# Kernel tuning notes

Hardware: AMD Instinct MI355X
Metric: run time of the kernel (lower is better)

Reference implementation:

```python
import jax, jax.numpy as jnp
import numpy as np


def setup_inputs() -> dict:
    key = jax.random.key(0)
    ks = jax.random.split(key, 12)
    B, N, Dv, E, H, V, T = 128, 196, 512, 512, 1024, 10000, 20
    s = 0.02  # small init scale for numerical stability
    f = lambda k, shp: (jax.random.normal(k, shp, jnp.float32) * s)
    return {
        "features": jax.random.normal(ks[0], (B, N, Dv), jnp.float32),
        "captions": jax.random.randint(ks[1], (B, T), 0, V),
        "W_init_h": f(ks[2], (H, Dv)),
        "W_init_c": f(ks[3], (H, Dv)),
        "W_attn_v": f(ks[4], (1, Dv)),
        "b_attn_v": jnp.zeros((1,), jnp.float32),
        "W_attn_h": f(ks[5], (1, H)),
        "b_attn_h": jnp.zeros((1,), jnp.float32),
        "embed_table": f(ks[6], (V, E)),
        "W_ih": f(ks[7], (4 * H, Dv + E)),
        "W_hh": f(ks[8], (4 * H, H)),
        "b_ih": jnp.zeros((4 * H,), jnp.float32),
        "b_hh": jnp.zeros((4 * H,), jnp.float32),
        "W_out": f(ks[9], (V, H)),
        "b_out": jnp.zeros((V,), jnp.float32),
    }


def reference(features, captions, W_init_h, W_init_c, W_attn_v, b_attn_v,
              W_attn_h, b_attn_h, embed_table, W_ih, W_hh, b_ih, b_hh,
              W_out, b_out):
    B, N, Dv = features.shape
    # _init_hidden: mean over vis_num of linear projections (division by vis_num)
    h0 = jnp.sum(jnp.einsum('bnd,hd->bnh', features, W_init_h), axis=1) / N
    c0 = jnp.sum(jnp.einsum('bnd,hd->bnh', features, W_init_c), axis=1) / N

    emb = embed_table[captions]                      # B,T,E
    emb_t_major = jnp.swapaxes(emb, 0, 1)            # T,B,E
    # visual attention logits are time-invariant; precompute once
    att_v = jnp.einsum('bnd,od->bno', features, W_attn_v) + b_attn_v  # B,N,1

    def step(carry, emb_t):
        h, c = carry
        # soft attention over vis_num locations
        att_h = (h @ W_attn_h.T + b_attn_h)[:, None, :]   # B,1,1
        alpha = jax.nn.softmax(att_v + att_h, axis=1)     # B,N,1
        ctx = jnp.sum(features * alpha, axis=1)           # B,Dv
        # single-step LSTM (PyTorch gate order: i, f, g, o)
        x = jnp.concatenate([ctx, emb_t], axis=-1)        # B,Dv+E
        gates = x @ W_ih.T + h @ W_hh.T + b_ih + b_hh     # B,4H
        i, fg, g, o = jnp.split(gates, 4, axis=-1)
        c_new = jax.nn.sigmoid(fg) * c + jax.nn.sigmoid(i) * jnp.tanh(g)
        h_new = jax.nn.sigmoid(o) * jnp.tanh(c_new)
        words = h_new @ W_out.T + b_out                   # B,V
        return (h_new, c_new), words

    _, word_space = jax.lax.scan(step, (h0, c0), emb_t_major)  # T,B,V
    # pack_padded_sequence with all-equal lengths flattens time-major -> (T*B, V)
    packed = word_space.reshape(-1, word_space.shape[-1])
    return jax.nn.log_softmax(packed, axis=1), jax.nn.softmax(packed, axis=1)
```

## Files before the change

kernel.cpp:

```cpp
#include <hip/hip_runtime.h>
#include <math.h>

#define B    128
#define NLOC 196
#define DV   512
#define EMB  512
#define HD   1024
#define VV   10000
#define TT   20
#define G4   4096
#define VPAD 10112
#define BH   (B*HD)

typedef short bf16x8 __attribute__((ext_vector_type(8)));
typedef float f32x4  __attribute__((ext_vector_type(4)));

__device__ __forceinline__ unsigned short f2bf(float x) {
    unsigned u = __builtin_bit_cast(unsigned, x);
    unsigned r = (u + 0x7fffu + ((u >> 16) & 1u)) >> 16;
    return (unsigned short)r;
}
__device__ __forceinline__ float bf2f(short s) {
    unsigned u = ((unsigned)(unsigned short)s) << 16;
    return __builtin_bit_cast(float, u);
}

__device__ __forceinline__ void gload_lds16(const void* g, void* lds) {
    __builtin_amdgcn_global_load_lds(
        (const __attribute__((address_space(1))) void*)g,
        (__attribute__((address_space(3))) void*)lds, 16, 0, 0);
}


__global__ void attv_kernel(const float* __restrict__ feat, const float* __restrict__ wv,
                            const float* __restrict__ bv, float* __restrict__ attv) {
    int row  = blockIdx.x;
    int lane = threadIdx.x;
    const float* p = feat + (size_t)row * DV;
    float s = 0.f;
    for (int k = lane; k < DV; k += 64) s += p[k] * wv[k];
    for (int off = 32; off > 0; off >>= 1) s += __shfl_down(s, off);
    if (lane == 0) attv[row] = s + bv[0];
}

__global__ void alpha_kernel(const float* __restrict__ attv, float* __restrict__ alpha) {
    int b   = blockIdx.x;
    int tid = threadIdx.x;
    __shared__ float red[256];
    float v = (tid < NLOC) ? attv[b * NLOC + tid] : -1e30f;
    red[tid] = v; __syncthreads();
    for (int s = 128; s > 0; s >>= 1) { if (tid < s) red[tid] = fmaxf(red[tid], red[tid + s]); __syncthreads(); }
    float m = red[0]; __syncthreads();
    float e = (tid < NLOC) ? expf(v - m) : 0.f;
    red[tid] = e; __syncthreads();
    for (int s = 128; s > 0; s >>= 1) { if (tid < s) red[tid] += red[tid + s]; __syncthreads(); }
    float sum = red[0];
    if (tid < NLOC) alpha[b * NLOC + tid] = e / sum;
}

__global__ void fmeanctx_kernel(const float* __restrict__ feat, const float* __restrict__ alpha,
                                short* __restrict__ fmean_b, short* __restrict__ ctx_b) {
    int idx = blockIdx.x * blockDim.x + threadIdx.x;
    if (idx >= B * DV) return;
    int b = idx / DV, d = idx % DV;
    const float* p = feat + (size_t)b * NLOC * DV + d;
    const float* a = alpha + b * NLOC;
    float sm = 0.f, sc = 0.f;
    for (int n = 0; n < NLOC; ++n) {
        float v = p[(size_t)n * DV];
        sm += v;
        sc += a[n] * v;
    }
    fmean_b[idx] = (short)f2bf(sm * (1.0f / NLOC));
    ctx_b[idx]   = (short)f2bf(sc);
}

__global__ void emb_gather_kernel(const int* __restrict__ captions, const float* __restrict__ table,
                                  short* __restrict__ emb_b) {
    size_t idx = (size_t)blockIdx.x * blockDim.x + threadIdx.x;
    if (idx >= (size_t)TT * B * EMB) return;
    int k = (int)(idx % EMB);
    int r = (int)(idx / EMB);
    int t = r / B, b = r % B;
    int cap = captions[b * TT + t];
    emb_b[idx] = (short)f2bf(table[(size_t)cap * EMB + k]);
}

__global__ void f2bf_pad_kernel(const float* __restrict__ in, short* __restrict__ out,
                                size_t n, size_t npad) {
    size_t i = (size_t)blockIdx.x * blockDim.x + threadIdx.x;
    if (i >= npad) return;
    out[i] = (i < n) ? (short)f2bf(in[i]) : (short)0;
}

__global__ void whh_perm_kernel(const float* __restrict__ in, short* __restrict__ out) {
    size_t idx = (size_t)blockIdx.x * blockDim.x + threadIdx.x;
    if (idx >= (size_t)G4 * HD) return;
    int k = (int)(idx & (HD - 1));
    int P = (int)(idx >> 10);
    int u = P >> 2, g = P & 3;
    out[idx] = (short)f2bf(in[(size_t)(g * HD + u) * HD + k]);
}

template<int BN, int WR, int WC, bool BF16OUT>
__global__ __launch_bounds__(256)
void gemm_bf16(const short* __restrict__ A, const short* __restrict__ Bw,
               void* __restrict__ C,
               const float* __restrict__ bias0, const float* __restrict__ bias1,
               int NY, int M, int N, int K, int lda, int ldb, int ldc) {
    constexpr int BM = 128;
    constexpr int BK = 32;
    constexpr int WM = BM / WR;
    constexpr int WN = BN / WC;
    constexpr int FM = WM / 16;
    constexpr int FN = WN / 16;
    __shared__ __align__(16) short As[BM * BK];
    __shared__ __align__(16) short Bs[BN * BK];
    const int tid  = threadIdx.x;
    const int wave = tid >> 6, lane = tid & 63;
    const int wr = wave / WC, wc = wave % WC;

    const int nwg = gridDim.x;
    const int qq = nwg >> 3, rr8 = nwg & 7;
    const int p = blockIdx.x;
    const int xcd = p & 7, slot = p >> 3;
    const int lwg = (xcd < rr8) ? (xcd * (qq + 1) + slot)
                                : (rr8 * (qq + 1) + (xcd - rr8) * qq + slot);
    const int m0 = (lwg % NY) * BM;
    const int n0 = (lwg / NY) * BN;
    const int laneoff = lane * 16;

    f32x4 acc[FM][FN] = {};

    for (int k0 = 0; k0 < K; k0 += BK) {
        #pragma unroll
        for (int r = 0; r < 2; ++r) {
            int o   = r * 4096 + wave * 1024 + laneoff;
            int row = o >> 6;
            int gr  = (o >> 4) & 3;
            int col = ((gr ^ ((row >> 1) & 3)) << 3);
            gload_lds16(A + (size_t)(m0 + row) * lda + k0 + col,
                        (char*)As + r * 4096 + wave * 1024);
        }
        constexpr int BBYTES = BN * BK * 2;
        if constexpr (BBYTES >= 4096) {
            #pragma unroll
            for (int r = 0; r < BBYTES / 4096; ++r) {
                int o   = r * 4096 + wave * 1024 + laneoff;
                int row = o >> 6;
                int gr  = (o >> 4) & 3;
                int col = ((gr ^ ((row >> 1) & 3)) << 3);
                gload_lds16(Bw + (size_t)(n0 + row) * ldb + k0 + col,
                            (char*)Bs + r * 4096 + wave * 1024);
            }
        } else {
            constexpr int NW = BBYTES / 1024;
            if (wave < NW) {
                int o   = wave * 1024 + laneoff;
                int row = o >> 6;
                int gr  = (o >> 4) & 3;
                int col = ((gr ^ ((row >> 1) & 3)) << 3);
                gload_lds16(Bw + (size_t)(n0 + row) * ldb + k0 + col,
                            (char*)Bs + wave * 1024);
            }
        }
        __syncthreads();

        bf16x8 a[FM], b[FN];
        const int kfrg = lane >> 4;
        #pragma unroll
        for (int i = 0; i < FM; ++i) {
            int row = wr * WM + i * 16 + (lane & 15);
            a[i] = *(const bf16x8*)&As[row * BK + ((kfrg ^ ((row >> 1) & 3)) << 3)];
        }
        #pragma unroll
        for (int j = 0; j < FN; ++j) {
            int row = wc * WN + j * 16 + (lane & 15);
            b[j] = *(const bf16x8*)&Bs[row * BK + ((kfrg ^ ((row >> 1) & 3)) << 3)];
        }
        #pragma unroll
        for (int i = 0; i < FM; ++i)
            #pragma unroll
            for (int j = 0; j < FN; ++j)
                acc[i][j] = __builtin_amdgcn_mfma_f32_16x16x32_bf16(a[i], b[j], acc[i][j], 0, 0, 0);
        __syncthreads();
    }

    #pragma unroll
    for (int i = 0; i < FM; ++i) {
        #pragma unroll
        for (int j = 0; j < FN; ++j) {
            int col = n0 + wc * WN + j * 16 + (lane & 15);
            if (col >= N) continue;
            float bv = (bias0 ? bias0[col] : 0.f) + (bias1 ? bias1[col] : 0.f);
            #pragma unroll
            for (int q = 0; q < 4; ++q) {
                int row = m0 + wr * WM + i * 16 + (lane >> 4) * 4 + q;
                if (row < M) {
                    float v = acc[i][j][q] + bv;
                    if constexpr (BF16OUT)
                        ((short*)C)[(size_t)row * ldc + col] = (short)f2bf(v);
                    else
                        ((float*)C)[(size_t)row * ldc + col] = v;
                }
            }
        }
    }
}

__global__ __launch_bounds__(256)
void gemm_k64(const short* __restrict__ A, const short* __restrict__ Bw,
              short* __restrict__ C,
              const float* __restrict__ bias0,
              int NY, int M, int N, int K, int lda, int ldb, int ldc) {
    __shared__ __align__(16) short As[128 * 64];
    __shared__ __align__(16) short Bs[128 * 64];
    const int tid  = threadIdx.x;
    const int wave = tid >> 6, lane = tid & 63;
    const int wr = wave >> 1, wc = wave & 1;

    const int nwg = gridDim.x;
    const int qq = nwg >> 3, rr8 = nwg & 7;
    const int p = blockIdx.x;
    const int xcd = p & 7, slot = p >> 3;
    const int lwg = (xcd < rr8) ? (xcd * (qq + 1) + slot)
                                : (rr8 * (qq + 1) + (xcd - rr8) * qq + slot);
    const int m0 = (lwg % NY) * 128;
    const int n0 = (lwg / NY) * 128;
    const int laneoff = lane * 16;
    const int kfrg = lane >> 4;

    f32x4 acc[4][4] = {};

    for (int k0 = 0; k0 < K; k0 += 64) {
        #pragma unroll
        for (int r = 0; r < 4; ++r) {
            int o   = r * 4096 + wave * 1024 + laneoff;
            int row = o >> 7;
            int gr  = (o >> 4) & 7;
            int col = ((gr ^ (row & 7)) << 3);
            gload_lds16(A + (size_t)(m0 + row) * lda + k0 + col,
                        (char*)As + r * 4096 + wave * 1024);
            gload_lds16(Bw + (size_t)(n0 + row) * ldb + k0 + col,
                        (char*)Bs + r * 4096 + wave * 1024);
        }
        __syncthreads();

        #pragma unroll
        for (int kh = 0; kh < 2; ++kh) {
            bf16x8 a[4], b[4];
            #pragma unroll
            for (int i = 0; i < 4; ++i) {
                int row = wr * 64 + i * 16 + (lane & 15);
                a[i] = *(const bf16x8*)&As[row * 64 + (((kh * 4 + kfrg) ^ (row & 7)) << 3)];
            }
            #pragma unroll
            for (int j = 0; j < 4; ++j) {
                int row = wc * 64 + j * 16 + (lane & 15);
                b[j] = *(const bf16x8*)&Bs[row * 64 + (((kh * 4 + kfrg) ^ (row & 7)) << 3)];
            }
            #pragma unroll
            for (int i = 0; i < 4; ++i)
                #pragma unroll
                for (int j = 0; j < 4; ++j)
                    acc[i][j] = __builtin_amdgcn_mfma_f32_16x16x32_bf16(a[i], b[j], acc[i][j], 0, 0, 0);
        }
        __syncthreads();
    }

    #pragma unroll
    for (int i = 0; i < 4; ++i) {
        #pragma unroll
        for (int j = 0; j < 4; ++j) {
            int col = n0 + wc * 64 + j * 16 + (lane & 15);
            if (col >= N) continue;
            float bv = bias0 ? bias0[col] : 0.f;
            #pragma unroll
            for (int q = 0; q < 4; ++q) {
                int row = m0 + wr * 64 + i * 16 + (lane >> 4) * 4 + q;
                if (row < M) C[(size_t)row * ldc + col] = (short)f2bf(acc[i][j][q] + bv);
            }
        }
    }
}

__global__ __launch_bounds__(256)
void lstm_step6(const short* __restrict__ Hprev, const short* __restrict__ Whh_p,
                const short* __restrict__ pre_t, const short* __restrict__ gctx_b,
                float* __restrict__ cbuf, short* __restrict__ Hnext,
                short* __restrict__ Hall_t) {
    __shared__ __align__(16) short As[64 * 512];
    __shared__ __align__(16) short Ws[32 * 512];
    __shared__ float gsm[4][64][8];
    const int tid  = threadIdx.x;
    const int lane = tid & 63, wave = tid >> 6;
    const int n0 = blockIdx.x * 32;
    const int m0 = blockIdx.y * 64;

    const int arowL = wave * 16 + (lane & 15);
    const int brow0 = lane & 15;
    const int brow1 = 16 + (lane & 15);
    const int kg    = lane >> 4;

    f32x4 acc0 = {}, acc1 = {};

    for (int h2 = 0; h2 < 2; ++h2) {
        const int k0 = h2 * 512;
        #pragma unroll
        for (int it = 0; it < 16; ++it) {
            int fg  = it * 256 + tid;
            int row = fg >> 6;
            int g   = fg & 63;
            int col = (g ^ (row & 7)) * 8;
            gload_lds16(Hprev + (size_t)(m0 + row) * HD + k0 + col,
                        (char*)As + it * 4096 + wave * 1024);
        }
        #pragma unroll
        for (int it = 0; it < 8; ++it) {
            int fg  = it * 256 + tid;
            int row = fg >> 6;
            int g   = fg & 63;
            int col = (g ^ (row & 7)) * 8;
            gload_lds16(Whh_p + (size_t)(n0 + row) * HD + k0 + col,
                        (char*)Ws + it * 4096 + wave * 1024);
        }
        __syncthreads();
        #pragma unroll
        for (int ks = 0; ks < 16; ++ks) {
            int lg = ks * 4 + kg;
            bf16x8 a  = *(const bf16x8*)((const char*)As + arowL * 1024 + ((lg ^ (arowL & 7)) << 4));
            bf16x8 w0 = *(const bf16x8*)((const char*)Ws + brow0 * 1024 + ((lg ^ (brow0 & 7)) << 4));
            bf16x8 w1 = *(const bf16x8*)((const char*)Ws + brow1 * 1024 + ((lg ^ (brow1 & 7)) << 4));
            acc0 = __builtin_amdgcn_mfma_f32_16x16x32_bf16(a, w0, acc0, 0, 0, 0);
            acc1 = __builtin_amdgcn_mfma_f32_16x16x32_bf16(a, w1, acc1, 0, 0, 0);
        }
        __syncthreads();
    }

    #pragma unroll
    for (int q = 0; q < 4; ++q) {
        int rr = wave * 16 + (lane >> 4) * 4 + q;
        gsm[brow0 & 3][rr][brow0 >> 2] = acc0[q];
        gsm[brow1 & 3][rr][brow1 >> 2] = acc1[q];
    }
    __syncthreads();

    #pragma unroll
    for (int s = 0; s < 2; ++s) {
        int idx = tid + s * 256;
        int m = idx >> 3, u8 = idx & 7;
        int r = m0 + m, u = blockIdx.x * 8 + u8;
        size_t pb = (size_t)r * G4 + u;
        float gi  = gsm[0][m][u8] + bf2f(pre_t[pb])          + bf2f(gctx_b[pb]);
        float gf  = gsm[1][m][u8] + bf2f(pre_t[pb + HD])     + bf2f(gctx_b[pb + HD]);
        float gg2 = gsm[2][m][u8] + bf2f(pre_t[pb + 2 * HD]) + bf2f(gctx_b[pb + 2 * HD]);
        float go  = gsm[3][m][u8] + bf2f(pre_t[pb + 3 * HD]) + bf2f(gctx_b[pb + 3 * HD]);
        float si = 1.f / (1.f + expf(-gi));
        float sf = 1.f / (1.f + expf(-gf));
        float so = 1.f / (1.f + expf(-go));
        float cn = sf * cbuf[(size_t)r * HD + u] + si * tanhf(gg2);
        float hn = so * tanhf(cn);
        cbuf[(size_t)r * HD + u] = cn;
        short hb = (short)f2bf(hn);
        Hnext[(size_t)r * HD + u]  = hb;
        Hall_t[(size_t)r * HD + u] = hb;
    }
}

__global__ __launch_bounds__(512)
void softmax_kernel(const short* __restrict__ wbf, float* __restrict__ logout,
                    float* __restrict__ smout) {
    __shared__ float rowbuf[VV];
    __shared__ float red[512];
    int r = blockIdx.x;
    int tid = threadIdx.x;
    const short* row = wbf + (size_t)r * VV;
    float m = -1e30f;
    for (int i = tid; i < VV; i += 512) {
        float v = bf2f(row[i]);
        rowbuf[i] = v;
        m = fmaxf(m, v);
    }
    red[tid] = m; __syncthreads();
    for (int s = 256; s > 0; s >>= 1) { if (tid < s) red[tid] = fmaxf(red[tid], red[tid + s]); __syncthreads(); }
    m = red[0]; __syncthreads();
    float sum = 0.f;
    for (int i = tid; i < VV; i += 512) sum += expf(rowbuf[i] - m);
    red[tid] = sum; __syncthreads();
    for (int s = 256; s > 0; s >>= 1) { if (tid < s) red[tid] += red[tid + s]; __syncthreads(); }
    sum = red[0];
    float inv = 1.f / sum;
    float lz = logf(sum);
    for (int i = tid; i < VV; i += 512) {
        float x = rowbuf[i];
        smout[(size_t)r * VV + i]  = expf(x - m) * inv;
        logout[(size_t)r * VV + i] = x - m - lz;
    }
}

extern "C" void kernel_launch(void* const* d_in, const int* in_sizes, int n_in,
                              void* d_out, int out_size, void* d_ws, size_t ws_size,
                              hipStream_t stream) {
    const float* features    = (const float*)d_in[0];
    const int*   captions    = (const int*)  d_in[1];
    const float* W_init_h    = (const float*)d_in[2];
    const float* W_init_c    = (const float*)d_in[3];
    const float* W_attn_v    = (const float*)d_in[4];
    const float* b_attn_v    = (const float*)d_in[5];
    const float* embed_table = (const float*)d_in[8];
    const float* W_ih        = (const float*)d_in[9];
    const float* W_hh        = (const float*)d_in[10];
    const float* b_ih        = (const float*)d_in[11];
    const float* b_hh        = (const float*)d_in[12];
    const float* W_out       = (const float*)d_in[13];
    const float* b_out       = (const float*)d_in[14];

    float* out   = (float*)d_out;
    float* words = out;
    float* s2    = out + (size_t)TT * B * VV;

    short* gate_pre_b = (short*)s2;
    short* Hall_b   = (short*)(s2 + (size_t)10485760);
    short* Wout_b   = (short*)(s2 + (size_t)10485760 + 1310720);
    short* Wih_b    = Wout_b + (size_t)VPAD * HD;
    short* Whh_b    = Wih_b  + (size_t)G4 * HD;
    short* Wini_h_b = Whh_b  + (size_t)G4 * HD;
    short* Wini_c_b = Wini_h_b + (size_t)HD * DV;

    char* w = (char*)d_ws;
    size_t off = 0;
    auto alloc = [&](size_t bytes) { void* p = w + off; off = (off + bytes + 255) & ~255UL; return p; };
    float* attv   = (float*)alloc((size_t)B * NLOC * 4);
    float* alpha  = (float*)alloc((size_t)B * NLOC * 4);
    short* gctx_b = (short*)alloc((size_t)B * G4 * 2);
    float* cbuf   = (float*)alloc((size_t)B * HD * 4);
    short* fmean_b= (short*)alloc((size_t)B * DV * 2);
    short* ctx_b  = (short*)alloc((size_t)B * DV * 2);
    short* h_ping = (short*)alloc((size_t)B * HD * 2);
    short* h_pong = (short*)alloc((size_t)B * HD * 2);
    short* emb_b  = (short*)alloc((size_t)TT * B * EMB * 2);
    short* words_bf = (short*)alloc((size_t)TT * B * VV * 2);

    f2bf_pad_kernel<<<((size_t)VPAD * HD + 255) / 256, 256, 0, stream>>>(
        W_out, Wout_b, (size_t)VV * HD, (size_t)VPAD * HD);
    f2bf_pad_kernel<<<((size_t)G4 * HD + 255) / 256, 256, 0, stream>>>(
        W_ih, Wih_b, (size_t)G4 * HD, (size_t)G4 * HD);
    whh_perm_kernel<<<((size_t)G4 * HD + 255) / 256, 256, 0, stream>>>(W_hh, Whh_b);
    f2bf_pad_kernel<<<((size_t)HD * DV + 255) / 256, 256, 0, stream>>>(
        W_init_h, Wini_h_b, (size_t)HD * DV, (size_t)HD * DV);
    f2bf_pad_kernel<<<((size_t)HD * DV + 255) / 256, 256, 0, stream>>>(
        W_init_c, Wini_c_b, (size_t)HD * DV, (size_t)HD * DV);

    attv_kernel<<<B * NLOC, 64, 0, stream>>>(features, W_attn_v, b_attn_v, attv);
    alpha_kernel<<<B, 256, 0, stream>>>(attv, alpha);
    fmeanctx_kernel<<<(B * DV + 255) / 256, 256, 0, stream>>>(features, alpha, fmean_b, ctx_b);
    emb_gather_kernel<<<((size_t)TT * B * EMB + 255) / 256, 256, 0, stream>>>(captions, embed_table, emb_b);

    gemm_bf16<32, 4, 1, true><<<dim3(HD / 32), 256, 0, stream>>>(
        fmean_b, Wini_h_b, h_ping, nullptr, nullptr, 1, B, HD, DV, DV, DV, HD);
    gemm_bf16<32, 4, 1, false><<<dim3(HD / 32), 256, 0, stream>>>(
        fmean_b, Wini_c_b, cbuf, nullptr, nullptr, 1, B, HD, DV, DV, DV, HD);

    gemm_bf16<32, 4, 1, true><<<dim3(G4 / 32), 256, 0, stream>>>(
        ctx_b, Wih_b, gctx_b, b_ih, b_hh, 1, B, G4, DV, DV, HD, G4);
    gemm_k64<<<dim3((G4 / 128) * (TT * B / 128)), 256, 0, stream>>>(
        emb_b, Wih_b + DV, gate_pre_b, nullptr, TT * B / 128,
        TT * B, G4, EMB, EMB, DV + EMB, G4);

    for (int t = 0; t < TT; ++t) {
        lstm_step6<<<dim3(G4 / 32, B / 64), 256, 0, stream>>>(
            (t & 1) ? h_pong : h_ping, Whh_b, gate_pre_b + (size_t)t * B * G4, gctx_b,
            cbuf, (t & 1) ? h_ping : h_pong, Hall_b + (size_t)t * BH);
    }

    gemm_k64<<<dim3((VPAD / 128) * (TT * B / 128)), 256, 0, stream>>>(
        Hall_b, Wout_b, words_bf, b_out, TT * B / 128,
        TT * B, VV, HD, HD, HD, VV);
    softmax_kernel<<<TT * B, 512, 0, stream>>>(words_bf, words, s2);
}
```

Measured before the change: 485.9 us.

## Shrink LSTM step tiles for more blocks and vectorize conversion kernels

The per-timestep LSTM kernel now uses 32x32 output tiles with K staged in four 256-wide chunks, so each wave owns one 16x16 fragment. This doubles the grid to 512 blocks and cuts LDS per block, which should fill the GPU better on the serial recurrent path. The cost is more reloading of W_hh and H across blocks and more barriers per step. Separately, the weight conversion, permutation and embedding gather kernels now process four floats per thread with vector loads and stores.

```diff
diff --git a/kernel.cpp b/kernel.cpp
--- a/kernel.cpp
+++ b/kernel.cpp
@@ -13,6 +13,7 @@
 #define BH   (B*HD)
 
 typedef short bf16x8 __attribute__((ext_vector_type(8)));
+typedef short s16x4  __attribute__((ext_vector_type(4)));
 typedef float f32x4  __attribute__((ext_vector_type(4)));
 
 __device__ __forceinline__ unsigned short f2bf(float x) {
@@ -77,29 +78,41 @@
 
 __global__ void emb_gather_kernel(const int* __restrict__ captions, const float* __restrict__ table,
                                   short* __restrict__ emb_b) {
-    size_t idx = (size_t)blockIdx.x * blockDim.x + threadIdx.x;
-    if (idx >= (size_t)TT * B * EMB) return;
+    size_t q = (size_t)blockIdx.x * blockDim.x + threadIdx.x;
+    if (q >= (size_t)TT * B * EMB / 4) return;
+    size_t idx = q * 4;
     int k = (int)(idx % EMB);
     int r = (int)(idx / EMB);
     int t = r / B, b = r % B;
     int cap = captions[b * TT + t];
-    emb_b[idx] = (short)f2bf(table[(size_t)cap * EMB + k]);
+    float4 v = *(const float4*)&table[(size_t)cap * EMB + k];
+    s16x4 o = { (short)f2bf(v.x), (short)f2bf(v.y), (short)f2bf(v.z), (short)f2bf(v.w) };
+    *(s16x4*)&emb_b[idx] = o;
 }
 
 __global__ void f2bf_pad_kernel(const float* __restrict__ in, short* __restrict__ out,
                                 size_t n, size_t npad) {
-    size_t i = (size_t)blockIdx.x * blockDim.x + threadIdx.x;
+    size_t q = (size_t)blockIdx.x * blockDim.x + threadIdx.x;
+    size_t i = q * 4;
     if (i >= npad) return;
-    out[i] = (i < n) ? (short)f2bf(in[i]) : (short)0;
+    s16x4 o = {0, 0, 0, 0};
+    if (i < n) {
+        float4 v = *(const float4*)&in[i];
+        o = s16x4{ (short)f2bf(v.x), (short)f2bf(v.y), (short)f2bf(v.z), (short)f2bf(v.w) };
+    }
+    *(s16x4*)&out[i] = o;
 }
 
 __global__ void whh_perm_kernel(const float* __restrict__ in, short* __restrict__ out) {
-    size_t idx = (size_t)blockIdx.x * blockDim.x + threadIdx.x;
-    if (idx >= (size_t)G4 * HD) return;
+    size_t q = (size_t)blockIdx.x * blockDim.x + threadIdx.x;
+    if (q >= (size_t)G4 * HD / 4) return;
+    size_t idx = q * 4;
     int k = (int)(idx & (HD - 1));
     int P = (int)(idx >> 10);
     int u = P >> 2, g = P & 3;
-    out[idx] = (short)f2bf(in[(size_t)(g * HD + u) * HD + k]);
+    float4 v = *(const float4*)&in[(size_t)(g * HD + u) * HD + k];
+    s16x4 o = { (short)f2bf(v.x), (short)f2bf(v.y), (short)f2bf(v.z), (short)f2bf(v.w) };
+    *(s16x4*)&out[idx] = o;
 }
 
 template<int BN, int WR, int WC, bool BF16OUT>
@@ -285,86 +298,72 @@
 }
 
 __global__ __launch_bounds__(256)
-void lstm_step6(const short* __restrict__ Hprev, const short* __restrict__ Whh_p,
+void lstm_step8(const short* __restrict__ Hprev, const short* __restrict__ Whh_p,
                 const short* __restrict__ pre_t, const short* __restrict__ gctx_b,
                 float* __restrict__ cbuf, short* __restrict__ Hnext,
                 short* __restrict__ Hall_t) {
-    __shared__ __align__(16) short As[64 * 512];
-    __shared__ __align__(16) short Ws[32 * 512];
-    __shared__ float gsm[4][64][8];
+    __shared__ __align__(16) short As[32 * 256];
+    __shared__ __align__(16) short Ws[32 * 256];
+    __shared__ float gsm[4][32][8];
     const int tid  = threadIdx.x;
     const int lane = tid & 63, wave = tid >> 6;
     const int n0 = blockIdx.x * 32;
-    const int m0 = blockIdx.y * 64;
-
-    const int arowL = wave * 16 + (lane & 15);
-    const int brow0 = lane & 15;
-    const int brow1 = 16 + (lane & 15);
+    const int m0 = blockIdx.y * 32;
+
+    const int mi = wave >> 1, ni = wave & 1;
+    const int arowL = mi * 16 + (lane & 15);
+    const int browL = ni * 16 + (lane & 15);
     const int kg    = lane >> 4;
 
-    f32x4 acc0 = {}, acc1 = {};
-
-    for (int h2 = 0; h2 < 2; ++h2) {
-        const int k0 = h2 * 512;
-        #pragma unroll
-        for (int it = 0; it < 16; ++it) {
+    f32x4 acc = {};
+
+    for (int qk = 0; qk < 4; ++qk) {
+        const int k0 = qk * 256;
+        #pragma unroll
+        for (int it = 0; it < 4; ++it) {
             int fg  = it * 256 + tid;
-            int row = fg >> 6;
-            int g   = fg & 63;
+            int row = fg >> 5;
+            int g   = fg & 31;
             int col = (g ^ (row & 7)) * 8;
             gload_lds16(Hprev + (size_t)(m0 + row) * HD + k0 + col,
                         (char*)As + it * 4096 + wave * 1024);
-        }
-        #pragma unroll
-        for (int it = 0; it < 8; ++it) {
-            int fg  = it * 256 + tid;
-            int row = fg >> 6;
-            int g   = fg & 63;
-            int col = (g ^ (row & 7)) * 8;
             gload_lds16(Whh_p + (size_t)(n0 + row) * HD + k0 + col,
                         (char*)Ws + it * 4096 + wave * 1024);
         }
         __syncthreads();
         #pragma unroll
-        for (int ks = 0; ks < 16; ++ks) {
+        for (int ks = 0; ks < 8; ++ks) {
             int lg = ks * 4 + kg;
-            bf16x8 a  = *(const bf16x8*)((const char*)As + arowL * 1024 + ((lg ^ (arowL & 7)) << 4));
-            bf16x8 w0 = *(const bf16x8*)((const char*)Ws + brow0 * 1024 + ((lg ^ (brow0 & 7)) << 4));
-            bf16x8 w1 = *(const bf16x8*)((const char*)Ws + brow1 * 1024 + ((lg ^ (brow1 & 7)) << 4));
-            acc0 = __builtin_amdgcn_mfma_f32_16x16x32_bf16(a, w0, acc0, 0, 0, 0);
-            acc1 = __builtin_amdgcn_mfma_f32_16x16x32_bf16(a, w1, acc1, 0, 0, 0);
+            bf16x8 a = *(const bf16x8*)((const char*)As + arowL * 512 + ((lg ^ (arowL & 7)) << 4));
+            bf16x8 w = *(const bf16x8*)((const char*)Ws + browL * 512 + ((lg ^ (browL & 7)) << 4));
+            acc = __builtin_amdgcn_mfma_f32_16x16x32_bf16(a, w, acc, 0, 0, 0);
         }
         __syncthreads();
     }
 
     #pragma unroll
     for (int q = 0; q < 4; ++q) {
-        int rr = wave * 16 + (lane >> 4) * 4 + q;
-        gsm[brow0 & 3][rr][brow0 >> 2] = acc0[q];
-        gsm[brow1 & 3][rr][brow1 >> 2] = acc1[q];
+        int rr = mi * 16 + (lane >> 4) * 4 + q;
+        gsm[browL & 3][rr][browL >> 2] = acc[q];
     }
     __syncthreads();
 
-    #pragma unroll
-    for (int s = 0; s < 2; ++s) {
-        int idx = tid + s * 256;
-        int m = idx >> 3, u8 = idx & 7;
-        int r = m0 + m, u = blockIdx.x * 8 + u8;
-        size_t pb = (size_t)r * G4 + u;
-        float gi  = gsm[0][m][u8] + bf2f(pre_t[pb])          + bf2f(gctx_b[pb]);
-        float gf  = gsm[1][m][u8] + bf2f(pre_t[pb + HD])     + bf2f(gctx_b[pb + HD]);
-        float gg2 = gsm[2][m][u8] + bf2f(pre_t[pb + 2 * HD]) + bf2f(gctx_b[pb + 2 * HD]);
-        float go  = gsm[3][m][u8] + bf2f(pre_t[pb + 3 * HD]) + bf2f(gctx_b[pb + 3 * HD]);
-        float si = 1.f / (1.f + expf(-gi));
-        float sf = 1.f / (1.f + expf(-gf));
-        float so = 1.f / (1.f + expf(-go));
-        float cn = sf * cbuf[(size_t)r * HD + u] + si * tanhf(gg2);
-        float hn = so * tanhf(cn);
-        cbuf[(size_t)r * HD + u] = cn;
-        short hb = (short)f2bf(hn);
-        Hnext[(size_t)r * HD + u]  = hb;
-        Hall_t[(size_t)r * HD + u] = hb;
-    }
+    const int m = tid >> 3, u8 = tid & 7;
+    const int r = m0 + m, u = blockIdx.x * 8 + u8;
+    size_t pb = (size_t)r * G4 + u;
+    float gi  = gsm[0][m][u8] + bf2f(pre_t[pb])          + bf2f(gctx_b[pb]);
+    float gf  = gsm[1][m][u8] + bf2f(pre_t[pb + HD])     + bf2f(gctx_b[pb + HD]);
+    float gg2 = gsm[2][m][u8] + bf2f(pre_t[pb + 2 * HD]) + bf2f(gctx_b[pb + 2 * HD]);
+    float go  = gsm[3][m][u8] + bf2f(pre_t[pb + 3 * HD]) + bf2f(gctx_b[pb + 3 * HD]);
+    float si = 1.f / (1.f + expf(-gi));
+    float sf = 1.f / (1.f + expf(-gf));
+    float so = 1.f / (1.f + expf(-go));
+    float cn = sf * cbuf[(size_t)r * HD + u] + si * tanhf(gg2);
+    float hn = so * tanhf(cn);
+    cbuf[(size_t)r * HD + u] = cn;
+    short hb = (short)f2bf(hn);
+    Hnext[(size_t)r * HD + u]  = hb;
+    Hall_t[(size_t)r * HD + u] = hb;
 }
 
 __global__ __launch_bounds__(512)
@@ -441,20 +440,21 @@
     short* emb_b  = (short*)alloc((size_t)TT * B * EMB * 2);
     short* words_bf = (short*)alloc((size_t)TT * B * VV * 2);
 
-    f2bf_pad_kernel<<<((size_t)VPAD * HD + 255) / 256, 256, 0, stream>>>(
+    f2bf_pad_kernel<<<((size_t)VPAD * HD / 4 + 255) / 256, 256, 0, stream>>>(
         W_out, Wout_b, (size_t)VV * HD, (size_t)VPAD * HD);
-    f2bf_pad_kernel<<<((size_t)G4 * HD + 255) / 256, 256, 0, stream>>>(
+    f2bf_pad_kernel<<<((size_t)G4 * HD / 4 + 255) / 256, 256, 0, stream>>>(
         W_ih, Wih_b, (size_t)G4 * HD, (size_t)G4 * HD);
-    whh_perm_kernel<<<((size_t)G4 * HD + 255) / 256, 256, 0, stream>>>(W_hh, Whh_b);
-    f2bf_pad_kernel<<<((size_t)HD * DV + 255) / 256, 256, 0, stream>>>(
+    whh_perm_kernel<<<((size_t)G4 * HD / 4 + 255) / 256, 256, 0, stream>>>(W_hh, Whh_b);
+    f2bf_pad_kernel<<<((size_t)HD * DV / 4 + 255) / 256, 256, 0, stream>>>(
         W_init_h, Wini_h_b, (size_t)HD * DV, (size_t)HD * DV);
-    f2bf_pad_kernel<<<((size_t)HD * DV + 255) / 256, 256, 0, stream>>>(
+    f2bf_pad_kernel<<<((size_t)HD * DV / 4 + 255) / 256, 256, 0, stream>>>(
         W_init_c, Wini_c_b, (size_t)HD * DV, (size_t)HD * DV);
 
     attv_kernel<<<B * NLOC, 64, 0, stream>>>(features, W_attn_v, b_attn_v, attv);
     alpha_kernel<<<B, 256, 0, stream>>>(attv, alpha);
     fmeanctx_kernel<<<(B * DV + 255) / 256, 256, 0, stream>>>(features, alpha, fmean_b, ctx_b);
-    emb_gather_kernel<<<((size_t)TT * B * EMB + 255) / 256, 256, 0, stream>>>(captions, embed_table, emb_b);
+    emb_gather_kernel<<<((size_t)TT * B * EMB / 4 + 255) / 256, 256, 0, stream>>>(
+        captions, embed_table, emb_b);
 
     gemm_bf16<32, 4, 1, true><<<dim3(HD / 32), 256, 0, stream>>>(
         fmean_b, Wini_h_b, h_ping, nullptr, nullptr, 1, B, HD, DV, DV, DV, HD);
@@ -468,7 +468,7 @@
         TT * B, G4, EMB, EMB, DV + EMB, G4);
 
     for (int t = 0; t < TT; ++t) {
-        lstm_step6<<<dim3(G4 / 32, B / 64), 256, 0, stream>>>(
+        lstm_step8<<<dim3(G4 / 32, B / 32), 256, 0, stream>>>(
             (t & 1) ? h_pong : h_ping, Whh_b, gate_pre_b + (size_t)t * B * G4, gctx_b,
             cbuf, (t & 1) ? h_ping : h_pong, Hall_b + (size_t)t * BH);
     }
```

After: 454.3 us. 6.5% less time.
